# Optimization experiments

Measured on AMD Instinct MI355X. Metric: run time of the kernel, lower is better.

Reference implementation:

```python
import jax, jax.numpy as jnp
import numpy as np

B, N, F, C = 8, 4096, 1024, 64


def setup_inputs() -> dict:
    key = jax.random.key(0)
    k1, k2, k3 = jax.random.split(key, 3)
    x1 = jax.random.normal(k1, (B, N, F), dtype=jnp.float32)
    x2 = jax.random.normal(k2, (B, N, F), dtype=jnp.float32)
    W = jax.random.normal(k3, (C, F), dtype=jnp.float32) / np.sqrt(F)
    b = jnp.zeros((C,), dtype=jnp.float32)
    return {"x1": x1, "x2": x2, "W": W, "b": b}


def _select_max(x, W, b):
    # x: [B, N, F] -> scores [B, N, C]
    scores = jnp.einsum("bnf,cf->bnc", x, W) + b
    # per-batch, per-class index of max-scoring instance: [B, C]
    idx = jnp.argmax(scores, axis=1)
    # gather the selected instance feature vectors: [B, C, F]
    return jnp.take_along_axis(x, idx[:, :, None], axis=1)


def reference(x1, x2, W, b):
    d = _select_max(x1, W, b)
    d1 = _select_max(x2, W, b)
    return (d, d1)
```

## Files before the change

### kernel.cpp

```cpp
#include <hip/hip_runtime.h>

#define B_   8
#define N_   4096
#define F_   1024
#define C_   64
#define ROWS 64
#define KC   32
#define NT   (F_ / KC)
#define NBLK (N_ / ROWS)
#define MARGIN 0.08f

typedef __attribute__((ext_vector_type(8))) short bhalf8;
typedef __attribute__((ext_vector_type(4))) float f32x4;
typedef __attribute__((ext_vector_type(4))) unsigned short us4;

__device__ __forceinline__ unsigned short f2bf_rne(float x) {
    unsigned u = __builtin_bit_cast(unsigned, x);
    u += 0x7fffu + ((u >> 16) & 1u);
    return (unsigned short)(u >> 16);
}
__device__ __forceinline__ bhalf8 cvt8(float4 a, float4 b) {
    bhalf8 r;
    r[0] = (short)f2bf_rne(a.x); r[1] = (short)f2bf_rne(a.y);
    r[2] = (short)f2bf_rne(a.z); r[3] = (short)f2bf_rne(a.w);
    r[4] = (short)f2bf_rne(b.x); r[5] = (short)f2bf_rne(b.y);
    r[6] = (short)f2bf_rne(b.z); r[7] = (short)f2bf_rne(b.w);
    return r;
}
__device__ __forceinline__ void load_lds16(const void* g, void* l) {
    __builtin_amdgcn_global_load_lds(
        (const __attribute__((address_space(1))) unsigned int*)g,
        (__attribute__((address_space(3))) unsigned int*)l, 16, 0, 0);
}

#define LEXGT(a, ai, b, bi) ((a) > (b) || ((a) == (b) && (ai) < (bi)))
#define INSERT3(vv, nn)                                                        \
    do {                                                                       \
        float _v = (vv); int _n = (nn);                                        \
        if (LEXGT(_v, _n, v0, i0)) { v2=v1; i2=i1; v1=v0; i1=i0; v0=_v; i0=_n; } \
        else if (LEXGT(_v, _n, v1, i1)) { v2=v1; i2=i1; v1=_v; i1=_n; }        \
        else if (LEXGT(_v, _n, v2, i2)) { v2=_v; i2=_n; }                      \
    } while (0)

__global__ __launch_bounds__(256) void wconv_kernel(
    const float* __restrict__ W, unsigned short* __restrict__ Wh)
{
    int i = blockIdx.x * 256 + threadIdx.x;
    float4 v = ((const float4*)W)[i];
    us4 hh;
    hh[0] = f2bf_rne(v.x); hh[1] = f2bf_rne(v.y);
    hh[2] = f2bf_rne(v.z); hh[3] = f2bf_rne(v.w);
    ((us4*)Wh)[i] = hh;
}

__global__ __launch_bounds__(256, 4) void score_top_kernel(
    const float* __restrict__ x1, const float* __restrict__ x2,
    const unsigned short* __restrict__ Wh,
    float* __restrict__ pv, int* __restrict__ pi)
{
    __shared__ __align__(16) char lds[24576];

    const int tid  = threadIdx.x;
    const int nb   = blockIdx.x;
    const int b    = blockIdx.y;
    const int inp  = blockIdx.z;
    const float* __restrict__ x = inp ? x2 : x1;
    const float* __restrict__ xbase = x + ((size_t)b * N_ + (size_t)nb * ROWS) * F_;

    const int lane = tid & 63;
    const int w    = tid >> 6;
    const int rsel = lane & 15;
    const int g    = lane >> 4;

    const int t0 = (nb ^ (b << 2) ^ (inp << 4)) & (NT - 1);

#define XOFF(buf) ((buf) * 8192)
#define WOFF(buf) (16384 + (buf) * 4096)

#define STAGE(t, buf)                                                          \
    do {                                                                       \
        const int f0_ = (t) * KC;                                              \
        _Pragma("unroll")                                                      \
        for (int j = 0; j < 2; ++j) {                                          \
            int ii = w * 2 + j;                                                \
            int r  = ii * 8 + (lane >> 3);                                     \
            int cg = (lane & 7) ^ (r & 7);                                     \
            load_lds16(xbase + (size_t)r * F_ + f0_ + cg * 4,                  \
                       lds + XOFF(buf) + ii * 1024);                           \
        }                                                                      \
        {                                                                      \
            int cls = w * 16 + (lane >> 2);                                    \
            int cg  = (lane & 3) ^ ((cls >> 1) & 3);                           \
            load_lds16(Wh + (size_t)cls * F_ + f0_ + cg * 8,                   \
                       lds + WOFF(buf) + w * 1024);                            \
        }                                                                      \
    } while (0)

#define COMPUTE(buf)                                                           \
    do {                                                                       \
        const char* xb = lds + XOFF(buf);                                      \
        const char* wb = lds + WOFF(buf);                                      \
        float4 xlo = *(const float4*)(xb + r_ * 128 + aswz0);                  \
        float4 xhi = *(const float4*)(xb + r_ * 128 + aswz1);                  \
        bhalf8 ah = cvt8(xlo, xhi);                                            \
        _Pragma("unroll")                                                      \
        for (int nt = 0; nt < 4; ++nt) {                                       \
            int cls = nt * 16 + rsel;                                          \
            bhalf8 bf = *(const bhalf8*)(wb + cls * 64 + ((g ^ ((cls >> 1) & 3)) * 16)); \
            acc[nt] = __builtin_amdgcn_mfma_f32_16x16x32_bf16(ah, bf, acc[nt], 0, 0, 0); \
        }                                                                      \
    } while (0)

    f32x4 acc[4];
    #pragma unroll
    for (int nt = 0; nt < 4; ++nt) acc[nt] = (f32x4){0.f, 0.f, 0.f, 0.f};

    const int r_    = w * 16 + rsel;
    const int aswz0 = ((2 * g)     ^ (r_ & 7)) * 16;
    const int aswz1 = ((2 * g + 1) ^ (r_ & 7)) * 16;

    STAGE(t0, 0);
    __syncthreads();

    for (int t = 0; t < NT; ++t) {
        const int cur = t & 1;
        if (t + 1 < NT) STAGE((t0 + t + 1) & (NT - 1), cur ^ 1);
        COMPUTE(cur);
        __syncthreads();
    }

    float wv0[4], wv1[4], wv2[4]; int wi0[4], wi1[4], wi2[4];
    #pragma unroll
    for (int nt = 0; nt < 4; ++nt) {
        float v0 = -3.4e38f, v1 = -3.4e38f, v2 = -3.4e38f;
        int   i0 = 0x7fffffff, i1 = 0x7fffffff, i2 = 0x7fffffff;
        #pragma unroll
        for (int r = 0; r < 4; ++r) {
            int n = nb * ROWS + w * 16 + 4 * g + r;
            INSERT3(acc[nt][r], n);
        }
        #pragma unroll
        for (int d = 16; d <= 32; d <<= 1) {
            float u0 = __shfl_xor(v0, d), u1 = __shfl_xor(v1, d), u2 = __shfl_xor(v2, d);
            int   j0 = __shfl_xor(i0, d), j1 = __shfl_xor(i1, d), j2 = __shfl_xor(i2, d);
            INSERT3(u0, j0); INSERT3(u1, j1); INSERT3(u2, j2);
        }
        wv0[nt] = v0; wv1[nt] = v1; wv2[nt] = v2;
        wi0[nt] = i0; wi1[nt] = i1; wi2[nt] = i2;
    }

    __syncthreads();
    float* tv = (float*)lds;
    int*   ti = (int*)(lds + 8192);
    if (lane < 16) {
        #pragma unroll
        for (int nt = 0; nt < 4; ++nt) {
            int c = nt * 16 + lane;
            tv[(w * C_ + c) * 3 + 0] = wv0[nt]; ti[(w * C_ + c) * 3 + 0] = wi0[nt];
            tv[(w * C_ + c) * 3 + 1] = wv1[nt]; ti[(w * C_ + c) * 3 + 1] = wi1[nt];
            tv[(w * C_ + c) * 3 + 2] = wv2[nt]; ti[(w * C_ + c) * 3 + 2] = wi2[nt];
        }
    }
    __syncthreads();

    if (tid < C_) {
        int c = tid;
        float v0 = -3.4e38f, v1 = -3.4e38f, v2 = -3.4e38f;
        int   i0 = 0x7fffffff, i1 = 0x7fffffff, i2 = 0x7fffffff;
        #pragma unroll
        for (int ww = 0; ww < 4; ++ww)
            #pragma unroll
            for (int k = 0; k < 3; ++k)
                INSERT3(tv[(ww * C_ + c) * 3 + k], ti[(ww * C_ + c) * 3 + k]);
        int blk = ((inp * B_ + b) * NBLK + nb);
        pv[(blk * C_ + c) * 3 + 0] = v0; pi[(blk * C_ + c) * 3 + 0] = i0;
        pv[(blk * C_ + c) * 3 + 1] = v1; pi[(blk * C_ + c) * 3 + 1] = i1;
        pv[(blk * C_ + c) * 3 + 2] = v2; pi[(blk * C_ + c) * 3 + 2] = i2;
    }
}

__global__ __launch_bounds__(64) void select_gather_kernel(
    const float* __restrict__ x1, const float* __restrict__ x2,
    const float* __restrict__ W,
    const float* __restrict__ pv, const int* __restrict__ pi,
    float* __restrict__ out)
{
    const int c    = blockIdx.x;
    const int b    = blockIdx.y;
    const int inp  = blockIdx.z;
    const int lane = threadIdx.x;

    const int blk  = ((inp * B_ + b) * NBLK + lane);
    const int base = (blk * C_ + c) * 3;
    const float v0 = pv[base + 0], v1 = pv[base + 1], v2 = pv[base + 2];
    const int   j0 = pi[base + 0], j1 = pi[base + 1], j2 = pi[base + 2];

    float m = v0;
    #pragma unroll
    for (int d = 32; d; d >>= 1) m = fmaxf(m, __shfl_xor(m, d));
    const float thr = m - MARGIN;

    int cand[8]; int nc = 0;
    #pragma unroll
    for (int k = 0; k < 3; ++k) {
        float vk = k == 0 ? v0 : (k == 1 ? v1 : v2);
        int   jk = k == 0 ? j0 : (k == 1 ? j1 : j2);
        unsigned long long mask = __ballot(vk >= thr);
        while (mask) {
            int l = __ffsll(mask) - 1; mask &= mask - 1;
            int n = __shfl(jk, l);
            if (nc < 8) cand[nc++] = n;
        }
    }

    const float* __restrict__ x = inp ? x2 : x1;
    int winner;
    if (nc == 1) {
        winner = cand[0];
    } else {
        float bv = -3.4e38f; int bn = 0x7fffffff;
        const float4* wrow = (const float4*)(W + (size_t)c * F_) + lane * 4;
        for (int k = 0; k < nc; ++k) {
            int n = cand[k];
            const float4* xrow = (const float4*)(x + ((size_t)b * N_ + n) * F_) + lane * 4;
            float p = 0.f;
            #pragma unroll
            for (int q = 0; q < 4; ++q) {
                float4 xv = xrow[q], wq = wrow[q];
                p += xv.x * wq.x + xv.y * wq.y + xv.z * wq.z + xv.w * wq.w;
            }
            #pragma unroll
            for (int d = 32; d; d >>= 1) p += __shfl_xor(p, d);
            if (p > bv || (p == bv && n < bn)) { bv = p; bn = n; }
        }
        winner = bn;
    }

    const float4* src = (const float4*)(x + ((size_t)b * N_ + winner) * F_);
    float4* dst = (float4*)(out + (((size_t)inp * B_ + b) * C_ + c) * F_);
    #pragma unroll
    for (int q = 0; q < 4; ++q) dst[lane + 64 * q] = src[lane + 64 * q];
}

extern "C" void kernel_launch(void* const* d_in, const int* in_sizes, int n_in,
                              void* d_out, int out_size, void* d_ws, size_t ws_size,
                              hipStream_t stream) {
    const float* x1 = (const float*)d_in[0];
    const float* x2 = (const float*)d_in[1];
    const float* W  = (const float*)d_in[2];

    unsigned short* Wh = (unsigned short*)d_ws;
    float* pv = (float*)((char*)d_ws + (size_t)C_ * F_ * sizeof(unsigned short));
    int*   pi = (int*)((char*)pv + (size_t)2 * B_ * NBLK * C_ * 3 * sizeof(float));

    wconv_kernel<<<C_ * F_ / 1024, 256, 0, stream>>>(W, Wh);
    dim3 g1(NBLK, B_, 2);
    score_top_kernel<<<g1, 256, 0, stream>>>(x1, x2, Wh, pv, pi);
    dim3 g2(C_, B_, 2);
    select_gather_kernel<<<g2, 64, 0, stream>>>(x1, x2, W, pv, pi, (float*)d_out);
}
```

Baseline: 65.62 us.

## Halve row tile, double K chunk, split waves over classes, keep top-2 candidates

The score kernel now processes 32 rows per block with a 64-wide K chunk per stage, using a 2x2 wave split over rows and classes. Per-block candidate lists shrink from top-3 to top-2, and the select kernel reads two blocks per lane to match. Launch bounds rise to 5 blocks per SM and LDS grows to 32KB. The goal is more blocks for occupancy and fewer sync iterations per block. The cost is twice as many reads of W per unit of x, a larger partial buffer, and a small risk of missing the true argmax when candidates are close.

```diff
diff --git a/kernel.cpp b/kernel.cpp
--- a/kernel.cpp
+++ b/kernel.cpp
@@ -4,8 +4,8 @@
 #define N_   4096
 #define F_   1024
 #define C_   64
-#define ROWS 64
-#define KC   32
+#define ROWS 32
+#define KC   64
 #define NT   (F_ / KC)
 #define NBLK (N_ / ROWS)
 #define MARGIN 0.08f
@@ -34,12 +34,11 @@
 }
 
 #define LEXGT(a, ai, b, bi) ((a) > (b) || ((a) == (b) && (ai) < (bi)))
-#define INSERT3(vv, nn)                                                        \
+#define INSERT2(vv, nn)                                                        \
     do {                                                                       \
         float _v = (vv); int _n = (nn);                                        \
-        if (LEXGT(_v, _n, v0, i0)) { v2=v1; i2=i1; v1=v0; i1=i0; v0=_v; i0=_n; } \
-        else if (LEXGT(_v, _n, v1, i1)) { v2=v1; i2=i1; v1=_v; i1=_n; }        \
-        else if (LEXGT(_v, _n, v2, i2)) { v2=_v; i2=_n; }                      \
+        if (LEXGT(_v, _n, v0, i0)) { v1=v0; i1=i0; v0=_v; i0=_n; }             \
+        else if (LEXGT(_v, _n, v1, i1)) { v1=_v; i1=_n; }                      \
     } while (0)
 
 __global__ __launch_bounds__(256) void wconv_kernel(
@@ -53,46 +52,51 @@
     ((us4*)Wh)[i] = hh;
 }
 
-__global__ __launch_bounds__(256, 4) void score_top_kernel(
+__global__ __launch_bounds__(256, 5) void score_top_kernel(
     const float* __restrict__ x1, const float* __restrict__ x2,
     const unsigned short* __restrict__ Wh,
     float* __restrict__ pv, int* __restrict__ pi)
 {
-    __shared__ __align__(16) char lds[24576];
+    __shared__ __align__(16) char lds[32768];
 
     const int tid  = threadIdx.x;
     const int nb   = blockIdx.x;
     const int b    = blockIdx.y;
     const int inp  = blockIdx.z;
     const float* __restrict__ x = inp ? x2 : x1;
-    const float* __restrict__ xbase = x + ((size_t)b * N_ + (size_t)nb * ROWS) * F_;
+    const char* __restrict__ xbase = (const char*)(x + ((size_t)b * N_ + (size_t)nb * ROWS) * F_);
+    const char* __restrict__ wbase = (const char*)Wh;
 
     const int lane = tid & 63;
     const int w    = tid >> 6;
+    const int wm   = w & 1;
+    const int wn   = w >> 1;
     const int rsel = lane & 15;
     const int g    = lane >> 4;
 
-    const int t0 = (nb ^ (b << 2) ^ (inp << 4)) & (NT - 1);
+    const int t0 = (nb ^ (b << 2) ^ (inp << 3)) & (NT - 1);
 
 #define XOFF(buf) ((buf) * 8192)
-#define WOFF(buf) (16384 + (buf) * 4096)
+#define WOFF(buf) (16384 + (buf) * 8192)
 
 #define STAGE(t, buf)                                                          \
     do {                                                                       \
-        const int f0_ = (t) * KC;                                              \
+        const int tb = (t);                                                    \
         _Pragma("unroll")                                                      \
-        for (int j = 0; j < 2; ++j) {                                          \
-            int ii = w * 2 + j;                                                \
-            int r  = ii * 8 + (lane >> 3);                                     \
-            int cg = (lane & 7) ^ (r & 7);                                     \
-            load_lds16(xbase + (size_t)r * F_ + f0_ + cg * 4,                  \
-                       lds + XOFF(buf) + ii * 1024);                           \
+        for (int j = 0; j < 2; ++j) {           \
+            int rb = w * 8 + j * 4;                                            \
+            int r  = rb + (lane >> 4);                                         \
+            int off = ((lane & 15) * 16) ^ ((r & 7) << 4);                     \
+            load_lds16(xbase + (size_t)r * 4096 + tb * 256 + off,              \
+                       lds + XOFF(buf) + rb * 256);                            \
         }                                                                      \
-        {                                                                      \
-            int cls = w * 16 + (lane >> 2);                                    \
-            int cg  = (lane & 3) ^ ((cls >> 1) & 3);                           \
-            load_lds16(Wh + (size_t)cls * F_ + f0_ + cg * 8,                   \
-                       lds + WOFF(buf) + w * 1024);                            \
+        _Pragma("unroll")                                                      \
+        for (int j = 0; j < 2; ++j) {            \
+            int ib  = w * 2 + j;                                               \
+            int cls = ib * 8 + (lane >> 3);                                    \
+            int off = ((lane & 7) * 16) ^ ((cls & 7) << 4);                    \
+            load_lds16(wbase + (size_t)cls * 2048 + tb * 128 + off,            \
+                       lds + WOFF(buf) + ib * 1024);                           \
         }                                                                      \
     } while (0)
 
@@ -100,24 +104,26 @@
     do {                                                                       \
         const char* xb = lds + XOFF(buf);                                      \
         const char* wb = lds + WOFF(buf);                                      \
-        float4 xlo = *(const float4*)(xb + r_ * 128 + aswz0);                  \
-        float4 xhi = *(const float4*)(xb + r_ * 128 + aswz1);                  \
-        bhalf8 ah = cvt8(xlo, xhi);                                            \
         _Pragma("unroll")                                                      \
-        for (int nt = 0; nt < 4; ++nt) {                                       \
-            int cls = nt * 16 + rsel;                                          \
-            bhalf8 bf = *(const bhalf8*)(wb + cls * 64 + ((g ^ ((cls >> 1) & 3)) * 16)); \
-            acc[nt] = __builtin_amdgcn_mfma_f32_16x16x32_bf16(ah, bf, acc[nt], 0, 0, 0); \
+        for (int ks = 0; ks < 2; ++ks) {                                       \
+            float4 xlo = *(const float4*)(xb + row_ * 256 + ((ks * 128 + g * 32)      ^ aswz)); \
+            float4 xhi = *(const float4*)(xb + row_ * 256 + ((ks * 128 + g * 32 + 16) ^ aswz)); \
+            bhalf8 ah = cvt8(xlo, xhi);                                        \
+            _Pragma("unroll")                                                  \
+            for (int ntl = 0; ntl < 2; ++ntl) {                                \
+                int cls = wn * 32 + ntl * 16 + rsel;                           \
+                bhalf8 bf = *(const bhalf8*)(wb + cls * 128 + ((ks * 64 + g * 16) ^ aswz)); \
+                acc[ntl] = __builtin_amdgcn_mfma_f32_16x16x32_bf16(ah, bf, acc[ntl], 0, 0, 0); \
+            }                                                                  \
         }                                                                      \
     } while (0)
 
-    f32x4 acc[4];
-    #pragma unroll
-    for (int nt = 0; nt < 4; ++nt) acc[nt] = (f32x4){0.f, 0.f, 0.f, 0.f};
-
-    const int r_    = w * 16 + rsel;
-    const int aswz0 = ((2 * g)     ^ (r_ & 7)) * 16;
-    const int aswz1 = ((2 * g + 1) ^ (r_ & 7)) * 16;
+    f32x4 acc[2];
+    acc[0] = (f32x4){0.f, 0.f, 0.f, 0.f};
+    acc[1] = (f32x4){0.f, 0.f, 0.f, 0.f};
+
+    const int row_ = wm * 16 + rsel;
+    const int aswz = (rsel & 7) << 4;
 
     STAGE(t0, 0);
     __syncthreads();
@@ -129,53 +135,51 @@
         __syncthreads();
     }
 
-    float wv0[4], wv1[4], wv2[4]; int wi0[4], wi1[4], wi2[4];
-    #pragma unroll
-    for (int nt = 0; nt < 4; ++nt) {
-        float v0 = -3.4e38f, v1 = -3.4e38f, v2 = -3.4e38f;
-        int   i0 = 0x7fffffff, i1 = 0x7fffffff, i2 = 0x7fffffff;
+    float wv0[2], wv1[2]; int wi0[2], wi1[2];
+    #pragma unroll
+    for (int ntl = 0; ntl < 2; ++ntl) {
+        float v0 = -3.4e38f, v1 = -3.4e38f;
+        int   i0 = 0x7fffffff, i1 = 0x7fffffff;
         #pragma unroll
         for (int r = 0; r < 4; ++r) {
-            int n = nb * ROWS + w * 16 + 4 * g + r;
-            INSERT3(acc[nt][r], n);
+            int n = nb * ROWS + wm * 16 + 4 * g + r;
+            INSERT2(acc[ntl][r], n);
         }
         #pragma unroll
         for (int d = 16; d <= 32; d <<= 1) {
-            float u0 = __shfl_xor(v0, d), u1 = __shfl_xor(v1, d), u2 = __shfl_xor(v2, d);
-            int   j0 = __shfl_xor(i0, d), j1 = __shfl_xor(i1, d), j2 = __shfl_xor(i2, d);
-            INSERT3(u0, j0); INSERT3(u1, j1); INSERT3(u2, j2);
-        }
-        wv0[nt] = v0; wv1[nt] = v1; wv2[nt] = v2;
-        wi0[nt] = i0; wi1[nt] = i1; wi2[nt] = i2;
+            float u0 = __shfl_xor(v0, d), u1 = __shfl_xor(v1, d);
+            int   j0 = __shfl_xor(i0, d), j1 = __shfl_xor(i1, d);
+            INSERT2(u0, j0); INSERT2(u1, j1);
+        }
+        wv0[ntl] = v0; wv1[ntl] = v1;
+        wi0[ntl] = i0; wi1[ntl] = i1;
     }
 
     __syncthreads();
     float* tv = (float*)lds;
-    int*   ti = (int*)(lds + 8192);
+    int*   ti = (int*)(lds + 4096);
     if (lane < 16) {
         #pragma unroll
-        for (int nt = 0; nt < 4; ++nt) {
-            int c = nt * 16 + lane;
-            tv[(w * C_ + c) * 3 + 0] = wv0[nt]; ti[(w * C_ + c) * 3 + 0] = wi0[nt];
-            tv[(w * C_ + c) * 3 + 1] = wv1[nt]; ti[(w * C_ + c) * 3 + 1] = wi1[nt];
-            tv[(w * C_ + c) * 3 + 2] = wv2[nt]; ti[(w * C_ + c) * 3 + 2] = wi2[nt];
+        for (int ntl = 0; ntl < 2; ++ntl) {
+            int c = wn * 32 + ntl * 16 + lane;
+            tv[(wm * C_ + c) * 2 + 0] = wv0[ntl]; ti[(wm * C_ + c) * 2 + 0] = wi0[ntl];
+            tv[(wm * C_ + c) * 2 + 1] = wv1[ntl]; ti[(wm * C_ + c) * 2 + 1] = wi1[ntl];
         }
     }
     __syncthreads();
 
     if (tid < C_) {
         int c = tid;
-        float v0 = -3.4e38f, v1 = -3.4e38f, v2 = -3.4e38f;
-        int   i0 = 0x7fffffff, i1 = 0x7fffffff, i2 = 0x7fffffff;
-        #pragma unroll
-        for (int ww = 0; ww < 4; ++ww)
+        float v0 = -3.4e38f, v1 = -3.4e38f;
+        int   i0 = 0x7fffffff, i1 = 0x7fffffff;
+        #pragma unroll
+        for (int ww = 0; ww < 2; ++ww)
             #pragma unroll
-            for (int k = 0; k < 3; ++k)
-                INSERT3(tv[(ww * C_ + c) * 3 + k], ti[(ww * C_ + c) * 3 + k]);
+            for (int k = 0; k < 2; ++k)
+                INSERT2(tv[(ww * C_ + c) * 2 + k], ti[(ww * C_ + c) * 2 + k]);
         int blk = ((inp * B_ + b) * NBLK + nb);
-        pv[(blk * C_ + c) * 3 + 0] = v0; pi[(blk * C_ + c) * 3 + 0] = i0;
-        pv[(blk * C_ + c) * 3 + 1] = v1; pi[(blk * C_ + c) * 3 + 1] = i1;
-        pv[(blk * C_ + c) * 3 + 2] = v2; pi[(blk * C_ + c) * 3 + 2] = i2;
+        pv[(blk * C_ + c) * 2 + 0] = v0; pi[(blk * C_ + c) * 2 + 0] = i0;
+        pv[(blk * C_ + c) * 2 + 1] = v1; pi[(blk * C_ + c) * 2 + 1] = i1;
     }
 }
 
@@ -190,25 +194,29 @@
     const int inp  = blockIdx.z;
     const int lane = threadIdx.x;
 
-    const int blk  = ((inp * B_ + b) * NBLK + lane);
-    const int base = (blk * C_ + c) * 3;
-    const float v0 = pv[base + 0], v1 = pv[base + 1], v2 = pv[base + 2];
-    const int   j0 = pi[base + 0], j1 = pi[base + 1], j2 = pi[base + 2];
-
-    float m = v0;
+    float v[4]; int id[4];
+    #pragma unroll
+    for (int j = 0; j < 2; ++j) {
+        int blk = ((inp * B_ + b) * NBLK + lane * 2 + j);
+        #pragma unroll
+        for (int k = 0; k < 2; ++k) {
+            int off = (blk * C_ + c) * 2 + k;
+            v[j * 2 + k] = pv[off]; id[j * 2 + k] = pi[off];
+        }
+    }
+
+    float m = fmaxf(fmaxf(v[0], v[1]), fmaxf(v[2], v[3]));
     #pragma unroll
     for (int d = 32; d; d >>= 1) m = fmaxf(m, __shfl_xor(m, d));
     const float thr = m - MARGIN;
 
     int cand[8]; int nc = 0;
     #pragma unroll
-    for (int k = 0; k < 3; ++k) {
-        float vk = k == 0 ? v0 : (k == 1 ? v1 : v2);
-        int   jk = k == 0 ? j0 : (k == 1 ? j1 : j2);
-        unsigned long long mask = __ballot(vk >= thr);
+    for (int k = 0; k < 4; ++k) {
+        unsigned long long mask = __ballot(v[k] >= thr);
         while (mask) {
             int l = __ffsll(mask) - 1; mask &= mask - 1;
-            int n = __shfl(jk, l);
+            int n = __shfl(id[k], l);
             if (nc < 8) cand[nc++] = n;
         }
     }
@@ -251,7 +259,7 @@
 
     unsigned short* Wh = (unsigned short*)d_ws;
     float* pv = (float*)((char*)d_ws + (size_t)C_ * F_ * sizeof(unsigned short));
-    int*   pi = (int*)((char*)pv + (size_t)2 * B_ * NBLK * C_ * 3 * sizeof(float));
+    int*   pi = (int*)((char*)pv + (size_t)2 * B_ * NBLK * C_ * 2 * sizeof(float));
 
     wconv_kernel<<<C_ * F_ / 1024, 256, 0, stream>>>(W, Wh);
     dim3 g1(NBLK, B_, 2);
```

Result: faster. 63.57 us, median of 2 (-3.1%).
